# Kernel optimization log

Hardware: AMD Instinct MI355X
Metric: run time of the kernel (lower is better)

The kernel has to match this reference:

```python
import jax, jax.numpy as jnp
import numpy as np

N_HEADS = 16

def rotate_half(x):
    x1, x2 = jnp.split(x, 2, axis=-1)
    return jnp.concatenate([-x2, x1], axis=-1)

def setup_inputs() -> dict:
    key = jax.random.key(0)
    ks = jax.random.split(key, 6)
    dim = 2048
    B, T = 4, 2048
    x = jax.random.normal(ks[0], (B, T, dim), dtype=jnp.float32)
    pos = jnp.arange(T, dtype=jnp.float32).reshape(T, 1, 1)
    def w(k):
        return jax.random.normal(k, (dim, dim), dtype=jnp.float32) * 0.02
    return {
        "x": x, "pos": pos,
        "wq_w": w(ks[1]), "wq_b": jnp.zeros((dim,), jnp.float32),
        "wk_w": w(ks[2]), "wk_b": jnp.zeros((dim,), jnp.float32),
        "wv_w": w(ks[3]), "wv_b": jnp.zeros((dim,), jnp.float32),
        "wo_w": w(ks[4]), "wo_b": jnp.zeros((dim,), jnp.float32),
    }

def reference(x, pos, wq_w, wq_b, wk_w, wk_b, wv_w, wv_b, wo_w, wo_b):
    B, T, dim = x.shape
    H = N_HEADS
    hd = dim // H
    q = (x @ wq_w.T + wq_b).reshape(B, T, H, hd)
    k = (x @ wk_w.T + wk_b).reshape(B, T, H, hd)
    v = (x @ wv_w.T + wv_b).reshape(B, T, H, hd)
    # RoPE: freq over half the head dim, sin/cos tiled to full head dim
    freq = 1.0 / (10000.0 ** (jnp.arange(0, hd, 2, dtype=jnp.float32) / hd))  # [hd/2]
    ang = pos * freq                      # [T,1,hd/2]
    sin = jnp.concatenate([jnp.sin(ang), jnp.sin(ang)], axis=-1)  # [T,1,hd]
    cos = jnp.concatenate([jnp.cos(ang), jnp.cos(ang)], axis=-1)  # [T,1,hd]
    q = q * cos + rotate_half(q) * sin
    k = k * cos + rotate_half(k) * sin
    # [B,H,T,hd]
    q = q.transpose(0, 2, 1, 3)
    k = k.transpose(0, 2, 1, 3)
    v = v.transpose(0, 2, 1, 3)
    scale = 1.0 / np.sqrt(hd).astype(np.float32)
    attn = jnp.einsum('bhqd,bhkd->bhqk', q, k) * scale  # [B,H,T,T]
    attn = jax.nn.softmax(attn, axis=-1)
    out = jnp.einsum('bhqk,bhkd->bhqd', attn, v)        # [B,H,T,hd]
    out = out.transpose(0, 2, 1, 3).reshape(B, T, dim)
    return out @ wo_w.T + wo_b
```

## Files before the change

kernel.cpp:

```cpp
#include <hip/hip_runtime.h>


using floatx4  = __attribute__((ext_vector_type(4))) float;
using short8   = __attribute__((ext_vector_type(8))) short;
using ushortx4 = __attribute__((ext_vector_type(4))) unsigned short;

#define DEVFN static __device__ __forceinline__

DEVFN unsigned short f2bf(float f) {
  unsigned u = __builtin_bit_cast(unsigned, f);
  u += 0x7fffu + ((u >> 16) & 1u);
  return (unsigned short)(u >> 16);
}
DEVFN float bf2f(unsigned short h) {
  return __builtin_bit_cast(float, ((unsigned)h) << 16);
}

DEVFN void async_cp16(const unsigned short* g, unsigned short* l) {
  __builtin_amdgcn_global_load_lds(
      (const __attribute__((address_space(1))) void*)g,
      (__attribute__((address_space(3))) void*)l,
      16, 0, 0);
}

__global__ __launch_bounds__(256) void cast_kernel(const float4* __restrict__ in,
                                                   ushortx4* __restrict__ out) {
  long u = (long)blockIdx.x * 256 + threadIdx.x;
  float4 v = in[u];
  out[u] = (ushortx4){f2bf(v.x), f2bf(v.y), f2bf(v.z), f2bf(v.w)};
}

__global__ __launch_bounds__(256) void rope_kernel(unsigned short* __restrict__ Q,
                                                   unsigned short* __restrict__ K,
                                                   const float* __restrict__ pos) {
  long idx = (long)blockIdx.x * 256 + threadIdx.x;
  unsigned short* arr = (idx >> 23) ? K : Q;
  long rem = idx & ((1L << 23) - 1);
  long row = rem >> 6;
  int j = (int)(rem & 63);
  int t = (int)(row & 2047);
  float ang = pos[t] * exp2f(-0.20762051f * (float)j);
  float s = sinf(ang), c = cosf(ang);
  unsigned short* base = arr + (row << 7);
  float x1 = bf2f(base[j]), x2 = bf2f(base[j + 64]);
  base[j]      = f2bf(x1 * c - x2 * s);
  base[j + 64] = f2bf(x2 * c + x1 * s);
}

template <int MODE>
__global__ __launch_bounds__(512, 2) void gemm_bt(const unsigned short* __restrict__ A,
                                                  const unsigned short* __restrict__ Bw,
                                                  const float* __restrict__ bias,
                                                  void* __restrict__ Cout) {
  constexpr int K = 2048;
  constexpr int NT = 64;
  __shared__ __align__(16) unsigned short lds[49152];
  const int tid = threadIdx.x;
  const int wave = tid >> 6, lane = tid & 63;
  const int ln15 = lane & 15, quad = lane >> 4;
  const int wm = wave >> 2, wn = wave & 3;
  const int bid = blockIdx.x;
  const int xcd = bid & 7, sl = bid >> 3;
  const int m0 = (xcd * 4 + (sl & 3)) * 256;
  const int n0 = (sl >> 2) * 256;

  const unsigned short* srcA0;
  const unsigned short* srcA1;
  const unsigned short* srcB0;
  const unsigned short* srcB1;
  {
    int u = tid;
    int L = u >> 3, cc = (u & 7) ^ (L & 7);
    int row = L * 2 + (cc >> 2), col = (cc & 3) * 8;
    srcA0 = A + (long)(m0 + row) * K + col;
    srcB0 = Bw + (long)(n0 + row) * K + col;
  }
  {
    int u = tid + 512;
    int L = u >> 3, cc = (u & 7) ^ (L & 7);
    int row = L * 2 + (cc >> 2), col = (cc & 3) * 8;
    srcA1 = A + (long)(m0 + row) * K + col;
    srcB1 = Bw + (long)(n0 + row) * K + col;
  }
  const int sdst = wave * 512;

#define STAGE_G(t, bufp)                                                \
  do {                                                                  \
    async_cp16(srcA0 + (long)(t) * 32, (bufp) + sdst);                  \
    async_cp16(srcA1 + (long)(t) * 32, (bufp) + 4096 + sdst);           \
    async_cp16(srcB0 + (long)(t) * 32, (bufp) + 8192 + sdst);           \
    async_cp16(srcB1 + (long)(t) * 32, (bufp) + 12288 + sdst);          \
  } while (0)

  int offA[8], offB[4];
#pragma unroll
  for (int mi = 0; mi < 8; ++mi) {
    int row = wm * 128 + mi * 16 + ln15;
    int line = row >> 1, cc = (row & 1) * 4 + quad;
    offA[mi] = line * 64 + (cc ^ (line & 7)) * 8;
  }
#pragma unroll
  for (int nj = 0; nj < 4; ++nj) {
    int row = wn * 64 + nj * 16 + ln15;
    int line = row >> 1, cc = (row & 1) * 4 + quad;
    offB[nj] = 8192 + line * 64 + (cc ^ (line & 7)) * 8;
  }

  floatx4 acc[8][4];
#pragma unroll
  for (int i = 0; i < 8; ++i)
#pragma unroll
    for (int j = 0; j < 4; ++j) acc[i][j] = (floatx4){0.f, 0.f, 0.f, 0.f};

  unsigned short* const bA0 = lds;
  unsigned short* const bA1 = lds + 16384;
  unsigned short* const bA2 = lds + 32768;

  STAGE_G(0, bA0);
  STAGE_G(1, bA1);
  asm volatile("s_waitcnt vmcnt(4)" ::: "memory");
  __builtin_amdgcn_s_barrier();

  int cb = 0;
  for (int t = 0; t < NT; ++t) {
    unsigned short* cur = (cb == 0) ? bA0 : ((cb == 1) ? bA1 : bA2);
    if (t < NT - 2) {
      int nb = cb ? cb - 1 : 2;
      unsigned short* nxt = (nb == 0) ? bA0 : ((nb == 1) ? bA1 : bA2);
      STAGE_G(t + 2, nxt);
    }
    short8 af[8], bf4[4];
#pragma unroll
    for (int mi = 0; mi < 8; ++mi) af[mi] = *(const short8*)(cur + offA[mi]);
#pragma unroll
    for (int nj = 0; nj < 4; ++nj) bf4[nj] = *(const short8*)(cur + offB[nj]);
    __builtin_amdgcn_s_setprio(1);
#pragma unroll
    for (int mi = 0; mi < 8; ++mi)
#pragma unroll
      for (int nj = 0; nj < 4; ++nj)
        acc[mi][nj] = __builtin_amdgcn_mfma_f32_16x16x32_bf16(af[mi], bf4[nj],
                                                              acc[mi][nj], 0, 0, 0);
    __builtin_amdgcn_s_setprio(0);
    if (t < NT - 2) {
      asm volatile("s_waitcnt vmcnt(4)" ::: "memory");
    } else if (t == NT - 2) {
      asm volatile("s_waitcnt vmcnt(0)" ::: "memory");
    }
    __builtin_amdgcn_s_barrier();
    cb = (cb == 2) ? 0 : cb + 1;
  }
#undef STAGE_G

  const int b_ = m0 >> 11;
  const int t0m = m0 & 2047;
  const int h0 = n0 >> 7;

  if (MODE == 0) {
#pragma unroll
    for (int rnd = 0; rnd < 2; ++rnd) {
      __syncthreads();
      if (wm == rnd) {
#pragma unroll
        for (int nj = 0; nj < 4; ++nj) {
          int nloc = wn * 64 + nj * 16 + ln15;
          float bv = bias[n0 + nloc];
#pragma unroll
          for (int mi = 0; mi < 8; ++mi)
#pragma unroll
            for (int r = 0; r < 4; ++r) {
              int tl = mi * 16 + quad * 4 + r;
              int phys = (nloc >> 3) ^ (tl & 15);
              lds[tl * 256 + phys * 8 + (nloc & 7)] = f2bf(acc[mi][nj][r] + bv);
            }
        }
      }
      __syncthreads();
#pragma unroll
      for (int j = 0; j < 8; ++j) {
        int u = j * 512 + tid;
        int tl = u >> 5, c = u & 31;
        int phys = c ^ (tl & 15);
        int h = h0 + (c >> 4);
        int tt = t0m + rnd * 128 + tl;
        *(short8*)((unsigned short*)Cout +
                   ((((long)(b_ * 16 + h)) << 11) + tt) * 128 + (c & 15) * 8) =
            *(const short8*)(lds + tl * 256 + phys * 8);
      }
    }
  } else if (MODE == 1) {
#pragma unroll
    for (int rnd = 0; rnd < 2; ++rnd) {
      __syncthreads();
      if (wm == rnd) {
#pragma unroll
        for (int nj = 0; nj < 4; ++nj) {
          int nloc = wn * 64 + nj * 16 + ln15;
          float bv = bias[n0 + nloc];
#pragma unroll
          for (int mi = 0; mi < 8; ++mi)
#pragma unroll
            for (int r = 0; r < 4; ++r) {
              int tl = mi * 16 + quad * 4 + r;
              int phys = (tl >> 3) ^ (nloc & 15);
              lds[nloc * 128 + phys * 8 + (tl & 7)] = f2bf(acc[mi][nj][r] + bv);
            }
        }
      }
      __syncthreads();
#pragma unroll
      for (int j = 0; j < 8; ++j) {
        int u = j * 512 + tid;
        int nloc = u >> 4, c = u & 15;
        int phys = c ^ (nloc & 15);
        int h = h0 + (nloc >> 7), d = nloc & 127;
        *(short8*)((unsigned short*)Cout +
                   ((((long)(b_ * 16 + h)) << 7) + d) * 2048 + t0m + rnd * 128 + c * 8) =
            *(const short8*)(lds + nloc * 128 + phys * 8);
      }
    }
  } else {
    float* lf = (float*)lds;
#pragma unroll
    for (int rnd = 0; rnd < 4; ++rnd) {
      __syncthreads();
      if (wm == (rnd >> 1)) {
#pragma unroll
        for (int nj = 0; nj < 4; ++nj) {
          int nloc = wn * 64 + nj * 16 + ln15;
          float bv = bias[n0 + nloc];
#pragma unroll
          for (int mh = 0; mh < 4; ++mh) {
            int mi = (rnd & 1) * 4 + mh;
#pragma unroll
            for (int r = 0; r < 4; ++r) {
              int tl = mh * 16 + quad * 4 + r;
              int phys = (nloc >> 2) ^ (tl & 15);
              lf[tl * 256 + phys * 4 + (nloc & 3)] = acc[mi][nj][r] + bv;
            }
          }
        }
      }
      __syncthreads();
#pragma unroll
      for (int j = 0; j < 8; ++j) {
        int u = j * 512 + tid;
        int tl = u >> 6, c = u & 63;
        int phys = c ^ (tl & 15);
        int m = m0 + rnd * 64 + tl;
        *(floatx4*)((float*)Cout + (long)m * 2048 + n0 + c * 4) =
            *(const floatx4*)(lf + tl * 256 + phys * 4);
      }
    }
  }
}

__global__ __launch_bounds__(512, 2) void flash_kernel(
    const unsigned short* __restrict__ Q,
    const unsigned short* __restrict__ Kmat,
    const unsigned short* __restrict__ Vt,
    unsigned short* __restrict__ Out) {
  constexpr int T = 2048;
  constexpr float SCALE = 0.08838834764831845f;
  __shared__ __align__(16) unsigned short lds[49152];

  const int tid = threadIdx.x;
  const int wave = tid >> 6, lane = tid & 63;
  const int ln15 = lane & 15, quad = lane >> 4;
  const int l7 = ln15 & 7;
  const int bid = blockIdx.x;
  const int xcd = bid & 7, sl = bid >> 3;
  const int bh = xcd * 8 + (sl >> 3);
  const int q0 = (sl & 7) * 256;

  const unsigned short* Qb = Q + (long)bh * T * 128;
  const unsigned short* Kb = Kmat + (long)bh * T * 128;
  const unsigned short* Vb = Vt + (long)bh * 128 * T;
  unsigned short* pw = lds + 32768 + wave * 2048;

  short8 qf[2][4];
#pragma unroll
  for (int mi = 0; mi < 2; ++mi)
#pragma unroll
    for (int ks = 0; ks < 4; ++ks)
      qf[mi][ks] = *(const short8*)(Qb + (long)(q0 + wave * 32 + mi * 16 + ln15) * 128 +
                                    ks * 32 + quad * 8);

#define STAGE_KV(t, kdst, vdst)                                                  \
  do {                                                                           \
    _Pragma("unroll") for (int j = 0; j < 2; ++j) {                              \
      int u = j * 512 + tid;                                                     \
      int row = u >> 4;                                                          \
      int c = (u & 15) ^ (row & 15);                                             \
      async_cp16(Kb + (long)((t) * 64 + row) * 128 + c * 8,                      \
                 (kdst) + (j * 512 + wave * 64) * 8);                            \
    }                                                                            \
    _Pragma("unroll") for (int j = 0; j < 2; ++j) {                              \
      int u = j * 512 + tid;                                                     \
      int row = u >> 3;                                                          \
      int c = (u & 7) ^ (row & 7);                                               \
      async_cp16(Vb + (long)row * T + (t) * 64 + c * 8,                          \
                 (vdst) + (j * 512 + wave * 64) * 8);                            \
    }                                                                            \
  } while (0)

  STAGE_KV(0, lds, lds + 16384);
  asm volatile("s_waitcnt vmcnt(0)" ::: "memory");
  __syncthreads();

  floatx4 oacc[2][8];
#pragma unroll
  for (int mi = 0; mi < 2; ++mi)
#pragma unroll
    for (int nj = 0; nj < 8; ++nj) oacc[mi][nj] = (floatx4){0.f, 0.f, 0.f, 0.f};
  float mst[2][4], lsp[2][4];
#pragma unroll
  for (int mi = 0; mi < 2; ++mi)
#pragma unroll
    for (int r = 0; r < 4; ++r) { mst[mi][r] = -1e30f; lsp[mi][r] = 0.f; }

  for (int t = 0; t < 32; ++t) {
    unsigned short* kc = lds + (t & 1) * 8192;
    unsigned short* vc = lds + 16384 + (t & 1) * 8192;
    if (t < 31) {
      unsigned short* kn = lds + ((t + 1) & 1) * 8192;
      unsigned short* vn = lds + 16384 + ((t + 1) & 1) * 8192;
      STAGE_KV(t + 1, kn, vn);
    }

    floatx4 sacc[2][4];
#pragma unroll
    for (int mi = 0; mi < 2; ++mi)
#pragma unroll
      for (int ni = 0; ni < 4; ++ni) sacc[mi][ni] = (floatx4){0.f, 0.f, 0.f, 0.f};
#pragma unroll
    for (int ks = 0; ks < 4; ++ks) {
      short8 bfr[4];
#pragma unroll
      for (int ni = 0; ni < 4; ++ni) {
        int row = ni * 16 + ln15;
        int phys = (ks * 4 + quad) ^ ln15;
        bfr[ni] = *(const short8*)(kc + row * 128 + phys * 8);
      }
      __builtin_amdgcn_s_setprio(1);
#pragma unroll
      for (int mi = 0; mi < 2; ++mi)
#pragma unroll
        for (int ni = 0; ni < 4; ++ni)
          sacc[mi][ni] = __builtin_amdgcn_mfma_f32_16x16x32_bf16(qf[mi][ks], bfr[ni],
                                                                 sacc[mi][ni], 0, 0, 0);
      __builtin_amdgcn_s_setprio(0);
    }

#pragma unroll
    for (int mi = 0; mi < 2; ++mi)
#pragma unroll
      for (int r = 0; r < 4; ++r) {
        float mx = fmaxf(fmaxf(sacc[mi][0][r], sacc[mi][1][r]),
                         fmaxf(sacc[mi][2][r], sacc[mi][3][r]));
#pragma unroll
        for (int off = 1; off < 16; off <<= 1) mx = fmaxf(mx, __shfl_xor(mx, off, 16));
        mx *= SCALE;
        float mold = mst[mi][r];
        float mnew = fmaxf(mold, mx);
        float alpha = __expf(mold - mnew);
        float rs = 0.f;
#pragma unroll
        for (int ni = 0; ni < 4; ++ni) {
          float p = __expf(sacc[mi][ni][r] * SCALE - mnew);
          sacc[mi][ni][r] = p;
          rs += p;
        }
        mst[mi][r] = mnew;
        lsp[mi][r] = lsp[mi][r] * alpha + rs;
#pragma unroll
        for (int nj = 0; nj < 8; ++nj) oacc[mi][nj][r] *= alpha;
      }

#pragma unroll
    for (int mi = 0; mi < 2; ++mi)
#pragma unroll
      for (int ni = 0; ni < 4; ++ni) {
        int cc = ni * 2 + (ln15 >> 3);
#pragma unroll
        for (int r = 0; r < 4; ++r) {
          int m = mi * 16 + quad * 4 + r;
          pw[m * 64 + (cc ^ (m & 7)) * 8 + l7] = f2bf(sacc[mi][ni][r]);
        }
      }

#pragma unroll
    for (int ks = 0; ks < 2; ++ks) {
      short8 af[2], bv[8];
#pragma unroll
      for (int mi = 0; mi < 2; ++mi) {
        int phys = (ks * 4 + quad) ^ l7;
        af[mi] = *(const short8*)(pw + (mi * 16 + ln15) * 64 + phys * 8);
      }
#pragma unroll
      for (int nj = 0; nj < 8; ++nj) {
        int row = nj * 16 + ln15;
        int phys = (ks * 4 + quad) ^ (row & 7);
        bv[nj] = *(const short8*)(vc + row * 64 + phys * 8);
      }
      __builtin_amdgcn_s_setprio(1);
#pragma unroll
      for (int mi = 0; mi < 2; ++mi)
#pragma unroll
        for (int nj = 0; nj < 8; ++nj)
          oacc[mi][nj] = __builtin_amdgcn_mfma_f32_16x16x32_bf16(af[mi], bv[nj],
                                                                 oacc[mi][nj], 0, 0, 0);
      __builtin_amdgcn_s_setprio(0);
    }

    asm volatile("s_waitcnt vmcnt(0)" ::: "memory");
    __syncthreads();
  }
#undef STAGE_KV

  float rinv[2][4];
#pragma unroll
  for (int mi = 0; mi < 2; ++mi)
#pragma unroll
    for (int r = 0; r < 4; ++r) {
      float l = lsp[mi][r];
#pragma unroll
      for (int off = 1; off < 16; off <<= 1) l += __shfl_xor(l, off, 16);
      rinv[mi][r] = 1.f / l;
    }
#pragma unroll
  for (int mi = 0; mi < 2; ++mi)
#pragma unroll
    for (int nj = 0; nj < 8; ++nj)
#pragma unroll
      for (int r = 0; r < 4; ++r)
        lds[(wave * 32 + mi * 16 + quad * 4 + r) * 128 + nj * 16 + ln15] =
            f2bf(oacc[mi][nj][r] * rinv[mi][r]);
  __syncthreads();
  const int b = bh >> 4, h = bh & 15;
  long obase = ((long)(b * T + q0) << 11) + h * 128;
#pragma unroll
  for (int j = 0; j < 8; ++j) {
    int u = j * 512 + tid;
    int r = u >> 4, c = u & 15;
    *(short8*)(Out + obase + ((long)r << 11) + c * 8) =
        *(const short8*)(lds + r * 128 + c * 8);
  }
}

extern "C" void kernel_launch(void* const* d_in, const int* in_sizes, int n_in,
                              void* d_out, int out_size, void* d_ws, size_t ws_size,
                              hipStream_t stream) {
  const float* x    = (const float*)d_in[0];
  const float* pos  = (const float*)d_in[1];
  const float* wq_w = (const float*)d_in[2];
  const float* wq_b = (const float*)d_in[3];
  const float* wk_w = (const float*)d_in[4];
  const float* wk_b = (const float*)d_in[5];
  const float* wv_w = (const float*)d_in[6];
  const float* wv_b = (const float*)d_in[7];
  const float* wo_w = (const float*)d_in[8];
  const float* wo_b = (const float*)d_in[9];

  unsigned short* xb  = (unsigned short*)d_ws;
  unsigned short* wqb = xb  + (1u << 24);
  unsigned short* wkb = wqb + (1u << 22);
  unsigned short* wvb = wkb + (1u << 22);
  unsigned short* wob = wvb + (1u << 22);
  unsigned short* qb  = wob + (1u << 22);
  unsigned short* kb  = qb  + (1u << 24);
  unsigned short* vtb = kb  + (1u << 24);
  unsigned short* ab  = vtb + (1u << 24);

  cast_kernel<<<16384, 256, 0, stream>>>((const float4*)x, (ushortx4*)xb);
  cast_kernel<<<4096, 256, 0, stream>>>((const float4*)wq_w, (ushortx4*)wqb);
  cast_kernel<<<4096, 256, 0, stream>>>((const float4*)wk_w, (ushortx4*)wkb);
  cast_kernel<<<4096, 256, 0, stream>>>((const float4*)wv_w, (ushortx4*)wvb);
  cast_kernel<<<4096, 256, 0, stream>>>((const float4*)wo_w, (ushortx4*)wob);

  gemm_bt<0><<<256, 512, 0, stream>>>(xb, wqb, wq_b, (void*)qb);
  gemm_bt<0><<<256, 512, 0, stream>>>(xb, wkb, wk_b, (void*)kb);
  gemm_bt<1><<<256, 512, 0, stream>>>(xb, wvb, wv_b, (void*)vtb);
  rope_kernel<<<65536, 256, 0, stream>>>(qb, kb, pos);
  flash_kernel<<<512, 512, 0, stream>>>(qb, kb, vtb, ab);
  gemm_bt<2><<<256, 512, 0, stream>>>(ab, wob, wo_b, d_out);
}
```

Measured before the change: 697.7 us.

## Split GEMM main loop into two phases interleaving LDS reads, prefetch, and MFMA

Restructures the inner K-loop of the projection GEMM into two half-phases. Each phase loads half the A fragments from LDS, issues part of the next-stage async global-to-LDS copies, waits and barriers, then runs half the MFMAs. The aim is to overlap memory issue with matrix work and lower the number of fragment registers live at once, in the style of a ping-pong schedule. In exchange each iteration now carries extra barriers and lgkmcnt waits, which could serialize the waves.

```diff
diff --git a/kernel.cpp b/kernel.cpp
--- a/kernel.cpp
+++ b/kernel.cpp
@@ -84,6 +84,30 @@
   }
   const int sdst = wave * 512;
 
+  int offA[8], offB[4];
+#pragma unroll
+  for (int mi = 0; mi < 8; ++mi) {
+    int row = wm * 128 + mi * 16 + ln15;
+    int line = row >> 1, cc = (row & 1) * 4 + quad;
+    offA[mi] = line * 64 + (cc ^ (line & 7)) * 8;
+  }
+#pragma unroll
+  for (int nj = 0; nj < 4; ++nj) {
+    int row = wn * 64 + nj * 16 + ln15;
+    int line = row >> 1, cc = (row & 1) * 4 + quad;
+    offB[nj] = 8192 + line * 64 + (cc ^ (line & 7)) * 8;
+  }
+
+  floatx4 acc[8][4];
+#pragma unroll
+  for (int i = 0; i < 8; ++i)
+#pragma unroll
+    for (int j = 0; j < 4; ++j) acc[i][j] = (floatx4){0.f, 0.f, 0.f, 0.f};
+
+  unsigned short* const bA0 = lds;
+  unsigned short* const bA1 = lds + 16384;
+  unsigned short* const bA2 = lds + 32768;
+
 #define STAGE_G(t, bufp)                                                \
   do {                                                                  \
     async_cp16(srcA0 + (long)(t) * 32, (bufp) + sdst);                  \
@@ -92,30 +116,6 @@
     async_cp16(srcB1 + (long)(t) * 32, (bufp) + 12288 + sdst);          \
   } while (0)
 
-  int offA[8], offB[4];
-#pragma unroll
-  for (int mi = 0; mi < 8; ++mi) {
-    int row = wm * 128 + mi * 16 + ln15;
-    int line = row >> 1, cc = (row & 1) * 4 + quad;
-    offA[mi] = line * 64 + (cc ^ (line & 7)) * 8;
-  }
-#pragma unroll
-  for (int nj = 0; nj < 4; ++nj) {
-    int row = wn * 64 + nj * 16 + ln15;
-    int line = row >> 1, cc = (row & 1) * 4 + quad;
-    offB[nj] = 8192 + line * 64 + (cc ^ (line & 7)) * 8;
-  }
-
-  floatx4 acc[8][4];
-#pragma unroll
-  for (int i = 0; i < 8; ++i)
-#pragma unroll
-    for (int j = 0; j < 4; ++j) acc[i][j] = (floatx4){0.f, 0.f, 0.f, 0.f};
-
-  unsigned short* const bA0 = lds;
-  unsigned short* const bA1 = lds + 16384;
-  unsigned short* const bA2 = lds + 32768;
-
   STAGE_G(0, bA0);
   STAGE_G(1, bA1);
   asm volatile("s_waitcnt vmcnt(4)" ::: "memory");
@@ -124,25 +124,52 @@
   int cb = 0;
   for (int t = 0; t < NT; ++t) {
     unsigned short* cur = (cb == 0) ? bA0 : ((cb == 1) ? bA1 : bA2);
-    if (t < NT - 2) {
-      int nb = cb ? cb - 1 : 2;
-      unsigned short* nxt = (nb == 0) ? bA0 : ((nb == 1) ? bA1 : bA2);
-      STAGE_G(t + 2, nxt);
-    }
-    short8 af[8], bf4[4];
-#pragma unroll
-    for (int mi = 0; mi < 8; ++mi) af[mi] = *(const short8*)(cur + offA[mi]);
+    int nb = cb ? cb - 1 : 2;
+    unsigned short* nxt = (nb == 0) ? bA0 : ((nb == 1) ? bA1 : bA2);
+    const bool pf = (t < NT - 2);
+
+    short8 af[4], bf4[4];
+#pragma unroll
+    for (int mi = 0; mi < 4; ++mi) af[mi] = *(const short8*)(cur + offA[mi]);
 #pragma unroll
     for (int nj = 0; nj < 4; ++nj) bf4[nj] = *(const short8*)(cur + offB[nj]);
+    if (pf) {
+      async_cp16(srcA0 + (long)(t + 2) * 32, nxt + sdst);
+      async_cp16(srcA1 + (long)(t + 2) * 32, nxt + 4096 + sdst);
+    }
+    __builtin_amdgcn_s_barrier();
+    asm volatile("s_waitcnt lgkmcnt(0)" ::: "memory");
+    __builtin_amdgcn_sched_barrier(0);
     __builtin_amdgcn_s_setprio(1);
 #pragma unroll
-    for (int mi = 0; mi < 8; ++mi)
+    for (int mi = 0; mi < 4; ++mi)
 #pragma unroll
       for (int nj = 0; nj < 4; ++nj)
         acc[mi][nj] = __builtin_amdgcn_mfma_f32_16x16x32_bf16(af[mi], bf4[nj],
                                                               acc[mi][nj], 0, 0, 0);
     __builtin_amdgcn_s_setprio(0);
-    if (t < NT - 2) {
+    __builtin_amdgcn_s_barrier();
+
+    short8 ag[4];
+#pragma unroll
+    for (int mi = 0; mi < 4; ++mi) ag[mi] = *(const short8*)(cur + offA[4 + mi]);
+    if (pf) {
+      async_cp16(srcB0 + (long)(t + 2) * 32, nxt + 8192 + sdst);
+      async_cp16(srcB1 + (long)(t + 2) * 32, nxt + 12288 + sdst);
+    }
+    __builtin_amdgcn_s_barrier();
+    asm volatile("s_waitcnt lgkmcnt(0)" ::: "memory");
+    __builtin_amdgcn_sched_barrier(0);
+    __builtin_amdgcn_s_setprio(1);
+#pragma unroll
+    for (int mi = 0; mi < 4; ++mi)
+#pragma unroll
+      for (int nj = 0; nj < 4; ++nj)
+        acc[4 + mi][nj] = __builtin_amdgcn_mfma_f32_16x16x32_bf16(ag[mi], bf4[nj],
+                                                                  acc[4 + mi][nj],
+                                                                  0, 0, 0);
+    __builtin_amdgcn_s_setprio(0);
+    if (pf) {
       asm volatile("s_waitcnt vmcnt(4)" ::: "memory");
     } else if (t == NT - 2) {
       asm volatile("s_waitcnt vmcnt(0)" ::: "memory");
```

New measurement: 702.1 us. Within noise of the previous version (+0.6%).

## Fuse QKV GEMMs into one launch with RoPE epilogue; lazy softmax rescale

Applied to the files above, without the earlier changes.

Merges the three Q/K/V projection GEMMs into a single 768-block launch and applies RoPE inside the Q/K epilogue, using a precomputed cos/sin table. This removes the separate RoPE pass, which read and rewrote Q and K through global memory, and cuts launch count. In the flash kernel, softmax moves to exp2 with a prescaled log2e constant and skips the running-max rescale unless the max grows past a threshold. That threshold lets unnormalized exponents reach up to about 2^11.5, which is safe in fp32 but enlarges intermediate values. The cos/sin table reuses the attention output buffer before flash overwrites it.

```diff
diff --git a/kernel.cpp b/kernel.cpp
--- a/kernel.cpp
+++ b/kernel.cpp
@@ -30,28 +30,212 @@
   out[u] = (ushortx4){f2bf(v.x), f2bf(v.y), f2bf(v.z), f2bf(v.w)};
 }
 
-__global__ __launch_bounds__(256) void rope_kernel(unsigned short* __restrict__ Q,
-                                                   unsigned short* __restrict__ K,
-                                                   const float* __restrict__ pos) {
-  long idx = (long)blockIdx.x * 256 + threadIdx.x;
-  unsigned short* arr = (idx >> 23) ? K : Q;
-  long rem = idx & ((1L << 23) - 1);
-  long row = rem >> 6;
-  int j = (int)(rem & 63);
-  int t = (int)(row & 2047);
+__global__ __launch_bounds__(256) void cs_table_kernel(const float* __restrict__ pos,
+                                                       float2* __restrict__ cst) {
+  int idx = blockIdx.x * 256 + threadIdx.x;
+  int t = idx >> 6, j = idx & 63;
   float ang = pos[t] * exp2f(-0.20762051f * (float)j);
-  float s = sinf(ang), c = cosf(ang);
-  unsigned short* base = arr + (row << 7);
-  float x1 = bf2f(base[j]), x2 = bf2f(base[j + 64]);
-  base[j]      = f2bf(x1 * c - x2 * s);
-  base[j + 64] = f2bf(x2 * c + x1 * s);
-}
-
-template <int MODE>
-__global__ __launch_bounds__(512, 2) void gemm_bt(const unsigned short* __restrict__ A,
+  cst[idx] = make_float2(cosf(ang), sinf(ang));
+}
+
+__global__ __launch_bounds__(512, 2) void qkv_gemm(
+    const unsigned short* __restrict__ A,
+    const unsigned short* __restrict__ Wq, const unsigned short* __restrict__ Wk,
+    const unsigned short* __restrict__ Wv,
+    const float* __restrict__ bq, const float* __restrict__ bk,
+    const float* __restrict__ bv,
+    unsigned short* __restrict__ Oq, unsigned short* __restrict__ Ok,
+    unsigned short* __restrict__ Ov,
+    const float2* __restrict__ cst) {
+  constexpr int K = 2048;
+  constexpr int NT = 64;
+  __shared__ __align__(16) unsigned short lds[49152];
+  const int tid = threadIdx.x;
+  const int wave = tid >> 6, lane = tid & 63;
+  const int ln15 = lane & 15, quad = lane >> 4;
+  const int wm = wave >> 2, wn = wave & 3;
+  const int bid = blockIdx.x;
+  const int g = bid >> 8;
+  const int b2 = bid & 255;
+  const unsigned short* Bw = (g == 0) ? Wq : (g == 1) ? Wk : Wv;
+  const float* bias = (g == 0) ? bq : (g == 1) ? bk : bv;
+  unsigned short* Cout = (g == 0) ? Oq : (g == 1) ? Ok : Ov;
+  const int xcd = b2 & 7, sl = b2 >> 3;
+  const int m0 = (xcd * 4 + (sl & 3)) * 256;
+  const int n0 = (sl >> 2) * 256;
+
+  const unsigned short *srcA0, *srcA1, *srcB0, *srcB1;
+  {
+    int u = tid;
+    int L = u >> 3, cc = (u & 7) ^ (L & 7);
+    int row = L * 2 + (cc >> 2), col = (cc & 3) * 8;
+    srcA0 = A + (long)(m0 + row) * K + col;
+    srcB0 = Bw + (long)(n0 + row) * K + col;
+  }
+  {
+    int u = tid + 512;
+    int L = u >> 3, cc = (u & 7) ^ (L & 7);
+    int row = L * 2 + (cc >> 2), col = (cc & 3) * 8;
+    srcA1 = A + (long)(m0 + row) * K + col;
+    srcB1 = Bw + (long)(n0 + row) * K + col;
+  }
+  const int sdst = wave * 512;
+
+#define STAGE_G(t, bufp)                                                \
+  do {                                                                  \
+    async_cp16(srcA0 + (long)(t) * 32, (bufp) + sdst);                  \
+    async_cp16(srcA1 + (long)(t) * 32, (bufp) + 4096 + sdst);           \
+    async_cp16(srcB0 + (long)(t) * 32, (bufp) + 8192 + sdst);           \
+    async_cp16(srcB1 + (long)(t) * 32, (bufp) + 12288 + sdst);          \
+  } while (0)
+
+  int offA[8], offB[4];
+#pragma unroll
+  for (int mi = 0; mi < 8; ++mi) {
+    int row = wm * 128 + mi * 16 + ln15;
+    int line = row >> 1, cc = (row & 1) * 4 + quad;
+    offA[mi] = line * 64 + (cc ^ (line & 7)) * 8;
+  }
+#pragma unroll
+  for (int nj = 0; nj < 4; ++nj) {
+    int row = wn * 64 + nj * 16 + ln15;
+    int line = row >> 1, cc = (row & 1) * 4 + quad;
+    offB[nj] = 8192 + line * 64 + (cc ^ (line & 7)) * 8;
+  }
+
+  floatx4 acc[8][4];
+#pragma unroll
+  for (int i = 0; i < 8; ++i)
+#pragma unroll
+    for (int j = 0; j < 4; ++j) acc[i][j] = (floatx4){0.f, 0.f, 0.f, 0.f};
+
+  unsigned short* const bA0 = lds;
+  unsigned short* const bA1 = lds + 16384;
+  unsigned short* const bA2 = lds + 32768;
+
+  STAGE_G(0, bA0);
+  STAGE_G(1, bA1);
+  asm volatile("s_waitcnt vmcnt(4)" ::: "memory");
+  __builtin_amdgcn_s_barrier();
+
+  int cb = 0;
+  for (int t = 0; t < NT; ++t) {
+    unsigned short* cur = (cb == 0) ? bA0 : ((cb == 1) ? bA1 : bA2);
+    if (t < NT - 2) {
+      int nb = cb ? cb - 1 : 2;
+      unsigned short* nxt = (nb == 0) ? bA0 : ((nb == 1) ? bA1 : bA2);
+      STAGE_G(t + 2, nxt);
+    }
+    short8 af[8], bf4[4];
+#pragma unroll
+    for (int mi = 0; mi < 8; ++mi) af[mi] = *(const short8*)(cur + offA[mi]);
+#pragma unroll
+    for (int nj = 0; nj < 4; ++nj) bf4[nj] = *(const short8*)(cur + offB[nj]);
+    __builtin_amdgcn_s_setprio(1);
+#pragma unroll
+    for (int mi = 0; mi < 8; ++mi)
+#pragma unroll
+      for (int nj = 0; nj < 4; ++nj)
+        acc[mi][nj] = __builtin_amdgcn_mfma_f32_16x16x32_bf16(af[mi], bf4[nj],
+                                                              acc[mi][nj], 0, 0, 0);
+    __builtin_amdgcn_s_setprio(0);
+    if (t < NT - 2) {
+      asm volatile("s_waitcnt vmcnt(4)" ::: "memory");
+    } else if (t == NT - 2) {
+      asm volatile("s_waitcnt vmcnt(0)" ::: "memory");
+    }
+    __builtin_amdgcn_s_barrier();
+    cb = (cb == 2) ? 0 : cb + 1;
+  }
+#undef STAGE_G
+
+  const int b_ = m0 >> 11;
+  const int t0m = m0 & 2047;
+  const int h0 = n0 >> 7;
+
+  if (g == 2) {
+#pragma unroll
+    for (int rnd = 0; rnd < 2; ++rnd) {
+      __syncthreads();
+      if (wm == rnd) {
+#pragma unroll
+        for (int nj = 0; nj < 4; ++nj) {
+          int nloc = wn * 64 + nj * 16 + ln15;
+          float bv = bias[n0 + nloc];
+#pragma unroll
+          for (int mi = 0; mi < 8; ++mi)
+#pragma unroll
+            for (int r = 0; r < 4; ++r) {
+              int tl = mi * 16 + quad * 4 + r;
+              int phys = (tl >> 3) ^ (nloc & 15);
+              lds[nloc * 128 + phys * 8 + (tl & 7)] = f2bf(acc[mi][nj][r] + bv);
+            }
+        }
+      }
+      __syncthreads();
+#pragma unroll
+      for (int j = 0; j < 8; ++j) {
+        int u = j * 512 + tid;
+        int nloc = u >> 4, c = u & 15;
+        int phys = c ^ (nloc & 15);
+        int h = h0 + (nloc >> 7), d = nloc & 127;
+        *(short8*)(Cout +
+                   ((((long)(b_ * 16 + h)) << 7) + d) * 2048 + t0m + rnd * 128 + c * 8) =
+            *(const short8*)(lds + nloc * 128 + phys * 8);
+      }
+    }
+  } else {
+#pragma unroll
+    for (int rnd = 0; rnd < 2; ++rnd) {
+      __syncthreads();
+      if (wm == rnd) {
+#pragma unroll
+        for (int nj = 0; nj < 4; ++nj) {
+          int nloc = wn * 64 + nj * 16 + ln15;
+          float bv = bias[n0 + nloc];
+#pragma unroll
+          for (int mi = 0; mi < 8; ++mi)
+#pragma unroll
+            for (int r = 0; r < 4; ++r) {
+              int tl = mi * 16 + quad * 4 + r;
+              int phys = (nloc >> 3) ^ (tl & 15);
+              lds[tl * 256 + phys * 8 + (nloc & 7)] = f2bf(acc[mi][nj][r] + bv);
+            }
+        }
+      }
+      __syncthreads();
+#pragma unroll
+      for (int j = 0; j < 8; ++j) {
+        int u = j * 512 + tid;
+        int tl = u >> 5, c = u & 31;
+        int phys = c ^ (tl & 15);
+        int hh = h0 + (c >> 4);
+        int tt = t0m + rnd * 128 + tl;
+        int cl = c & 15;
+        int cp = (cl < 8) ? c + 8 : c - 8;
+        int physp = cp ^ (tl & 15);
+        short8 s8 = *(const short8*)(lds + tl * 256 + phys * 8);
+        short8 p8 = *(const short8*)(lds + tl * 256 + physp * 8);
+        const float2* ct = cst + tt * 64 + (cl & 7) * 8;
+        short8 o8;
+#pragma unroll
+        for (int e = 0; e < 8; ++e) {
+          float2 cs = ct[e];
+          float x = bf2f((unsigned short)s8[e]);
+          float y = bf2f((unsigned short)p8[e]);
+          float v = (cl < 8) ? (x * cs.x - y * cs.y) : (x * cs.x + y * cs.y);
+          o8[e] = (short)f2bf(v);
+        }
+        *(short8*)(Cout + ((((long)(b_ * 16 + hh)) << 11) + tt) * 128 + cl * 8) = o8;
+      }
+    }
+  }
+}
+
+__global__ __launch_bounds__(512, 2) void gemm_wo(const unsigned short* __restrict__ A,
                                                   const unsigned short* __restrict__ Bw,
                                                   const float* __restrict__ bias,
-                                                  void* __restrict__ Cout) {
+                                                  float* __restrict__ Cout) {
   constexpr int K = 2048;
   constexpr int NT = 64;
   __shared__ __align__(16) unsigned short lds[49152];
@@ -64,10 +248,7 @@
   const int m0 = (xcd * 4 + (sl & 3)) * 256;
   const int n0 = (sl >> 2) * 256;
 
-  const unsigned short* srcA0;
-  const unsigned short* srcA1;
-  const unsigned short* srcB0;
-  const unsigned short* srcB1;
+  const unsigned short *srcA0, *srcA1, *srcB0, *srcB1;
   {
     int u = tid;
     int L = u >> 3, cc = (u & 7) ^ (L & 7);
@@ -152,105 +333,36 @@
   }
 #undef STAGE_G
 
-  const int b_ = m0 >> 11;
-  const int t0m = m0 & 2047;
-  const int h0 = n0 >> 7;
-
-  if (MODE == 0) {
-#pragma unroll
-    for (int rnd = 0; rnd < 2; ++rnd) {
-      __syncthreads();
-      if (wm == rnd) {
-#pragma unroll
-        for (int nj = 0; nj < 4; ++nj) {
-          int nloc = wn * 64 + nj * 16 + ln15;
-          float bv = bias[n0 + nloc];
-#pragma unroll
-          for (int mi = 0; mi < 8; ++mi)
-#pragma unroll
-            for (int r = 0; r < 4; ++r) {
-              int tl = mi * 16 + quad * 4 + r;
-              int phys = (nloc >> 3) ^ (tl & 15);
-              lds[tl * 256 + phys * 8 + (nloc & 7)] = f2bf(acc[mi][nj][r] + bv);
-            }
-        }
-      }
-      __syncthreads();
-#pragma unroll
-      for (int j = 0; j < 8; ++j) {
-        int u = j * 512 + tid;
-        int tl = u >> 5, c = u & 31;
-        int phys = c ^ (tl & 15);
-        int h = h0 + (c >> 4);
-        int tt = t0m + rnd * 128 + tl;
-        *(short8*)((unsigned short*)Cout +
-                   ((((long)(b_ * 16 + h)) << 11) + tt) * 128 + (c & 15) * 8) =
-            *(const short8*)(lds + tl * 256 + phys * 8);
-      }
-    }
-  } else if (MODE == 1) {
-#pragma unroll
-    for (int rnd = 0; rnd < 2; ++rnd) {
-      __syncthreads();
-      if (wm == rnd) {
-#pragma unroll
-        for (int nj = 0; nj < 4; ++nj) {
-          int nloc = wn * 64 + nj * 16 + ln15;
-          float bv = bias[n0 + nloc];
-#pragma unroll
-          for (int mi = 0; mi < 8; ++mi)
-#pragma unroll
-            for (int r = 0; r < 4; ++r) {
-              int tl = mi * 16 + quad * 4 + r;
-              int phys = (tl >> 3) ^ (nloc & 15);
-              lds[nloc * 128 + phys * 8 + (tl & 7)] = f2bf(acc[mi][nj][r] + bv);
-            }
-        }
-      }
-      __syncthreads();
-#pragma unroll
-      for (int j = 0; j < 8; ++j) {
-        int u = j * 512 + tid;
-        int nloc = u >> 4, c = u & 15;
-        int phys = c ^ (nloc & 15);
-        int h = h0 + (nloc >> 7), d = nloc & 127;
-        *(short8*)((unsigned short*)Cout +
-                   ((((long)(b_ * 16 + h)) << 7) + d) * 2048 + t0m + rnd * 128 + c * 8) =
-            *(const short8*)(lds + nloc * 128 + phys * 8);
-      }
-    }
-  } else {
-    float* lf = (float*)lds;
-#pragma unroll
-    for (int rnd = 0; rnd < 4; ++rnd) {
-      __syncthreads();
-      if (wm == (rnd >> 1)) {
-#pragma unroll
-        for (int nj = 0; nj < 4; ++nj) {
-          int nloc = wn * 64 + nj * 16 + ln15;
-          float bv = bias[n0 + nloc];
-#pragma unroll
-          for (int mh = 0; mh < 4; ++mh) {
-            int mi = (rnd & 1) * 4 + mh;
-#pragma unroll
-            for (int r = 0; r < 4; ++r) {
-              int tl = mh * 16 + quad * 4 + r;
-              int phys = (nloc >> 2) ^ (tl & 15);
-              lf[tl * 256 + phys * 4 + (nloc & 3)] = acc[mi][nj][r] + bv;
-            }
+  float* lf = (float*)lds;
+#pragma unroll
+  for (int rnd = 0; rnd < 4; ++rnd) {
+    __syncthreads();
+    if (wm == (rnd >> 1)) {
+#pragma unroll
+      for (int nj = 0; nj < 4; ++nj) {
+        int nloc = wn * 64 + nj * 16 + ln15;
+        float bv = bias[n0 + nloc];
+#pragma unroll
+        for (int mh = 0; mh < 4; ++mh) {
+          int mi = (rnd & 1) * 4 + mh;
+#pragma unroll
+          for (int r = 0; r < 4; ++r) {
+            int tl = mh * 16 + quad * 4 + r;
+            int phys = (nloc >> 2) ^ (tl & 15);
+            lf[tl * 256 + phys * 4 + (nloc & 3)] = acc[mi][nj][r] + bv;
           }
         }
       }
-      __syncthreads();
-#pragma unroll
-      for (int j = 0; j < 8; ++j) {
-        int u = j * 512 + tid;
-        int tl = u >> 6, c = u & 63;
-        int phys = c ^ (tl & 15);
-        int m = m0 + rnd * 64 + tl;
-        *(floatx4*)((float*)Cout + (long)m * 2048 + n0 + c * 4) =
-            *(const floatx4*)(lf + tl * 256 + phys * 4);
-      }
+    }
+    __syncthreads();
+#pragma unroll
+    for (int j = 0; j < 8; ++j) {
+      int u = j * 512 + tid;
+      int tl = u >> 6, c = u & 63;
+      int phys = c ^ (tl & 15);
+      int m = m0 + rnd * 64 + tl;
+      *(floatx4*)(Cout + (long)m * 2048 + n0 + c * 4) =
+          *(const floatx4*)(lf + tl * 256 + phys * 4);
     }
   }
 }
@@ -261,7 +373,7 @@
     const unsigned short* __restrict__ Vt,
     unsigned short* __restrict__ Out) {
   constexpr int T = 2048;
-  constexpr float SCALE = 0.08838834764831845f;
+  constexpr float SL2E = 0.12754228f;
   __shared__ __align__(16) unsigned short lds[49152];
 
   const int tid = threadIdx.x;
@@ -360,21 +472,25 @@
                          fmaxf(sacc[mi][2][r], sacc[mi][3][r]));
 #pragma unroll
         for (int off = 1; off < 16; off <<= 1) mx = fmaxf(mx, __shfl_xor(mx, off, 16));
-        mx *= SCALE;
+        float mxs = mx * SL2E;
         float mold = mst[mi][r];
-        float mnew = fmaxf(mold, mx);
-        float alpha = __expf(mold - mnew);
+        if (!__all(mxs - mold <= 11.5f)) {
+          float mnew = fmaxf(mold, mxs);
+          float alpha = exp2f(mold - mnew);
+          lsp[mi][r] *= alpha;
+#pragma unroll
+          for (int nj = 0; nj < 8; ++nj) oacc[mi][nj][r] *= alpha;
+          mst[mi][r] = mnew;
+          mold = mnew;
+        }
         float rs = 0.f;
 #pragma unroll
         for (int ni = 0; ni < 4; ++ni) {
-          float p = __expf(sacc[mi][ni][r] * SCALE - mnew);
+          float p = exp2f(sacc[mi][ni][r] * SL2E - mold);
           sacc[mi][ni][r] = p;
           rs += p;
         }
-        mst[mi][r] = mnew;
-        lsp[mi][r] = lsp[mi][r] * alpha + rs;
-#pragma unroll
-        for (int nj = 0; nj < 8; ++nj) oacc[mi][nj][r] *= alpha;
+        lsp[mi][r] += rs;
       }
 
 #pragma unroll
@@ -471,17 +587,17 @@
   unsigned short* kb  = qb  + (1u << 24);
   unsigned short* vtb = kb  + (1u << 24);
   unsigned short* ab  = vtb + (1u << 24);
+  float2* cst = (float2*)ab;
 
   cast_kernel<<<16384, 256, 0, stream>>>((const float4*)x, (ushortx4*)xb);
   cast_kernel<<<4096, 256, 0, stream>>>((const float4*)wq_w, (ushortx4*)wqb);
   cast_kernel<<<4096, 256, 0, stream>>>((const float4*)wk_w, (ushortx4*)wkb);
   cast_kernel<<<4096, 256, 0, stream>>>((const float4*)wv_w, (ushortx4*)wvb);
   cast_kernel<<<4096, 256, 0, stream>>>((const float4*)wo_w, (ushortx4*)wob);
-
-  gemm_bt<0><<<256, 512, 0, stream>>>(xb, wqb, wq_b, (void*)qb);
-  gemm_bt<0><<<256, 512, 0, stream>>>(xb, wkb, wk_b, (void*)kb);
-  gemm_bt<1><<<256, 512, 0, stream>>>(xb, wvb, wv_b, (void*)vtb);
-  rope_kernel<<<65536, 256, 0, stream>>>(qb, kb, pos);
+  cs_table_kernel<<<512, 256, 0, stream>>>(pos, cst);
+
+  qkv_gemm<<<768, 512, 0, stream>>>(xb, wqb, wkb, wvb, wq_b, wk_b, wv_b,
+                                    qb, kb, vtb, cst);
   flash_kernel<<<512, 512, 0, stream>>>(qb, kb, vtb, ab);
-  gemm_bt<2><<<256, 512, 0, stream>>>(ab, wob, wo_b, d_out);
-}
+  gemm_wo<<<256, 512, 0, stream>>>(ab, wob, wo_b, (float*)d_out);
+}
```

After: 698.0 us. About the same (+0.0%).
